# Performance work log

Measured on AMD Instinct MI355X. Metric: run time of the kernel, lower is better.

## Reference

```python
import jax, jax.numpy as jnp
import numpy as np

BEV_RANGE = 32.0   # meters; traj xy normalized to [-1,1] by this half-range
NUM_HEADS = 8
EGO_FUT_TS = 8
EPS = 1e-5


def _ln(x, g, b):
    m = x.mean(-1, keepdims=True)
    v = ((x - m) ** 2).mean(-1, keepdims=True)
    return (x - m) / jnp.sqrt(v + EPS) * g + b


def _mha(q, k, v, wq, bq, wk, bk, wv, bv, wo, bo):
    B, Lq, D = q.shape
    Lk = k.shape[1]
    dh = D // NUM_HEADS
    qh = (q @ wq + bq).reshape(B, Lq, NUM_HEADS, dh).transpose(0, 2, 1, 3)
    kh = (k @ wk + bk).reshape(B, Lk, NUM_HEADS, dh).transpose(0, 2, 1, 3)
    vh = (v @ wv + bv).reshape(B, Lk, NUM_HEADS, dh).transpose(0, 2, 1, 3)
    a = jax.nn.softmax(jnp.einsum('bhqd,bhkd->bhqk', qh, kh) * (1.0 / float(np.sqrt(dh))), axis=-1)
    o = jnp.einsum('bhqk,bhkd->bhqd', a, vh).transpose(0, 2, 1, 3).reshape(B, Lq, D)
    return o @ wo + bo


def _grid_sample(value, grid):
    # value (B,C,H,W); grid (B,M,P,2) xy in [-1,1]; bilinear, zeros padding, align_corners=False
    B, C, H, W = value.shape
    x = (grid[..., 0] + 1.0) * (W * 0.5) - 0.5
    y = (grid[..., 1] + 1.0) * (H * 0.5) - 0.5
    x0 = jnp.floor(x)
    y0 = jnp.floor(y)
    bidx = jnp.arange(B)[:, None, None]

    def corner(xi, yi, w):
        valid = (xi >= 0) & (xi <= W - 1) & (yi >= 0) & (yi <= H - 1)
        xc = jnp.clip(xi, 0, W - 1).astype(jnp.int32)
        yc = jnp.clip(yi, 0, H - 1).astype(jnp.int32)
        v = value[bidx, :, yc, xc]  # advanced idx -> (B,M,P,C)
        return v * (w * valid)[..., None]

    return (corner(x0, y0, (x0 + 1 - x) * (y0 + 1 - y))
            + corner(x0 + 1, y0, (x - x0) * (y0 + 1 - y))
            + corner(x0, y0 + 1, (x0 + 1 - x) * (y - y0))
            + corner(x0 + 1, y0 + 1, (x - x0) * (y - y0)))


def _mish(x):
    return x * jnp.tanh(jax.nn.softplus(x))


def _forward(traj_feature, noisy_traj_points, bev_feature, agents_query, ego_query,
             time_embed, status_encoding,
             bev_value_w, bev_value_b, bev_attn_w, bev_attn_b, bev_out_w, bev_out_b,
             aq_wq, aq_bq, aq_wk, aq_bk, aq_wv, aq_bv, aq_wo, aq_bo,
             eq_wq, eq_bq, eq_wk, eq_bk, eq_wv, eq_bv, eq_wo, eq_bo,
             ffn_w1, ffn_b1, ffn_w2, ffn_b2,
             n1_g, n1_b, n2_g, n2_b, n3_g, n3_b,
             mod_w, mod_b,
             cls_w1, cls_b1, cls_ln1_g, cls_ln1_b, cls_w2, cls_b2, cls_ln2_g, cls_ln2_b, cls_w3, cls_b3,
             reg_w1, reg_b1, reg_w2, reg_b2, reg_w3, reg_b3):
    B, M, D = traj_feature.shape
    # --- GridSampleCrossBEVAttention ---
    value = jnp.einsum('bchw,cd->bdhw', bev_feature, bev_value_w) + bev_value_b[None, :, None, None]
    grid = noisy_traj_points / BEV_RANGE                    # (B,M,P,2) in [-1,1]
    sampled = _grid_sample(value, grid)                     # (B,M,P,D)
    pt_w = jax.nn.softmax(traj_feature @ bev_attn_w + bev_attn_b, axis=-1)  # (B,M,P)
    bev_out = jnp.einsum('bmpd,bmp->bmd', sampled, pt_w) @ bev_out_w + bev_out_b
    traj = traj_feature + bev_out
    # --- cross-agent attention + norm1 ---
    traj = _ln(traj + _mha(traj, agents_query, agents_query,
                           aq_wq, aq_bq, aq_wk, aq_bk, aq_wv, aq_bv, aq_wo, aq_bo), n1_g, n1_b)
    # --- cross-ego attention + norm2 ---
    traj = _ln(traj + _mha(traj, ego_query, ego_query,
                           eq_wq, eq_bq, eq_wk, eq_bk, eq_wv, eq_bv, eq_wo, eq_bo), n2_g, n2_b)
    # --- FFN + norm3 (note: no residual, matches source) ---
    traj = _ln(jax.nn.relu(traj @ ffn_w1 + ffn_b1) @ ffn_w2 + ffn_b2, n3_g, n3_b)
    # --- FiLM time modulation ---
    ss = _mish(time_embed) @ mod_w + mod_b                  # (B,1,2D)
    scale, shift = jnp.split(ss, 2, axis=-1)
    traj = traj * (1.0 + scale) + shift
    # --- task decoder: cls branch (linear_relu_ln x2 + Linear->1) ---
    h = _ln(jax.nn.relu(traj @ cls_w1 + cls_b1), cls_ln1_g, cls_ln1_b)
    h = _ln(jax.nn.relu(h @ cls_w2 + cls_b2), cls_ln2_g, cls_ln2_b)
    plan_cls = (h @ cls_w3 + cls_b3)[..., 0]                # (B,M)
    # --- task decoder: reg branch ---
    r = jax.nn.relu(traj @ reg_w1 + reg_b1)
    r = jax.nn.relu(r @ reg_w2 + reg_b2)
    r = (r @ reg_w3 + reg_b3).reshape(B, M, EGO_FUT_TS, 3)
    xy = r[..., :2] + noisy_traj_points
    heading = jnp.tanh(r[..., 2:3]) * np.pi
    poses_reg = jnp.concatenate([xy, heading], axis=-1)     # (B,M,T,3)
    return poses_reg, plan_cls


def setup_inputs() -> dict:
    key = jax.random.key(0)
    ks = iter(jax.random.split(key, 80))
    rn = lambda *s: jax.random.normal(next(ks), s, dtype=jnp.float32)
    w = lambda *s: rn(*s) * 0.05
    B, M, P, D, A, FF = 32, 20, 8, 256, 32, 1024
    inp = dict(
        traj_feature=rn(B, M, D),
        noisy_traj_points=rn(B, M, P, 2) * 8.0,
        bev_feature=rn(B, 256, 128, 128),
        agents_query=rn(B, A, D),
        ego_query=rn(B, 1, D),
        time_embed=rn(B, 1, D),
        status_encoding=rn(B, 1, D),
        bev_value_w=w(256, D), bev_value_b=jnp.zeros(D),
        bev_attn_w=w(D, P), bev_attn_b=jnp.zeros(P),
        bev_out_w=w(D, D), bev_out_b=jnp.zeros(D),
        aq_wq=w(D, D), aq_bq=jnp.zeros(D), aq_wk=w(D, D), aq_bk=jnp.zeros(D),
        aq_wv=w(D, D), aq_bv=jnp.zeros(D), aq_wo=w(D, D), aq_bo=jnp.zeros(D),
        eq_wq=w(D, D), eq_bq=jnp.zeros(D), eq_wk=w(D, D), eq_bk=jnp.zeros(D),
        eq_wv=w(D, D), eq_bv=jnp.zeros(D), eq_wo=w(D, D), eq_bo=jnp.zeros(D),
        ffn_w1=w(D, FF), ffn_b1=jnp.zeros(FF), ffn_w2=w(FF, D), ffn_b2=jnp.zeros(D),
        n1_g=jnp.ones(D), n1_b=jnp.zeros(D), n2_g=jnp.ones(D), n2_b=jnp.zeros(D),
        n3_g=jnp.ones(D), n3_b=jnp.zeros(D),
        mod_w=w(D, 2 * D), mod_b=jnp.zeros(2 * D),
        cls_w1=w(D, D), cls_b1=jnp.zeros(D), cls_ln1_g=jnp.ones(D), cls_ln1_b=jnp.zeros(D),
        cls_w2=w(D, D), cls_b2=jnp.zeros(D), cls_ln2_g=jnp.ones(D), cls_ln2_b=jnp.zeros(D),
        cls_w3=w(D, 1), cls_b3=jnp.full((1,), float(-np.log((1 - 0.01) / 0.01))),
        reg_w1=w(D, D), reg_b1=jnp.zeros(D), reg_w2=w(D, D), reg_b2=jnp.zeros(D),
        reg_w3=w(D, EGO_FUT_TS * 3), reg_b3=jnp.zeros(EGO_FUT_TS * 3),
        bev_spatial_shape=jnp.array([128, 128], dtype=jnp.int32),
    )
    return inp


def reference(traj_feature, noisy_traj_points, bev_feature, agents_query, ego_query,
              time_embed, status_encoding,
              bev_value_w, bev_value_b, bev_attn_w, bev_attn_b, bev_out_w, bev_out_b,
              aq_wq, aq_bq, aq_wk, aq_bk, aq_wv, aq_bv, aq_wo, aq_bo,
              eq_wq, eq_bq, eq_wk, eq_bk, eq_wv, eq_bv, eq_wo, eq_bo,
              ffn_w1, ffn_b1, ffn_w2, ffn_b2,
              n1_g, n1_b, n2_g, n2_b, n3_g, n3_b,
              mod_w, mod_b,
              cls_w1, cls_b1, cls_ln1_g, cls_ln1_b, cls_w2, cls_b2, cls_ln2_g, cls_ln2_b, cls_w3, cls_b3,
              reg_w1, reg_b1, reg_w2, reg_b2, reg_w3, reg_b3,
              bev_spatial_shape):
    # bev_spatial_shape is implied by bev_feature's static shape under jit
    return _forward(traj_feature, noisy_traj_points, bev_feature, agents_query, ego_query,
                    time_embed, status_encoding,
                    bev_value_w, bev_value_b, bev_attn_w, bev_attn_b, bev_out_w, bev_out_b,
                    aq_wq, aq_bq, aq_wk, aq_bk, aq_wv, aq_bv, aq_wo, aq_bo,
                    eq_wq, eq_bq, eq_wk, eq_bk, eq_wv, eq_bv, eq_wo, eq_bo,
                    ffn_w1, ffn_b1, ffn_w2, ffn_b2,
                    n1_g, n1_b, n2_g, n2_b, n3_g, n3_b,
                    mod_w, mod_b,
                    cls_w1, cls_b1, cls_ln1_g, cls_ln1_b, cls_w2, cls_b2, cls_ln2_g, cls_ln2_b, cls_w3, cls_b3,
                    reg_w1, reg_b1, reg_w2, reg_b2, reg_w3, reg_b3)
```

## Files before the change

### kernel.cpp

```cpp
#include <hip/hip_runtime.h>
#include <math.h>

constexpr int NB = 32;
constexpr int NM = 20;
constexpr int NP = 8;
constexpr int ND = 256;
constexpr int NA = 32;
constexpr int NFF = 1024;
constexpr int NH = 128, NW = 128;
constexpr int HW = NH * NW;

constexpr int PK_BVW = 0;
constexpr int PK_BOW = 65536;
constexpr int PK_WQ  = 131072;
constexpr int PK_WO  = 196608;
constexpr int PK_CW1 = 262144;
constexpr int PK_CW2 = 327680;
constexpr int PK_RW1 = 393216;
constexpr int PK_RW2 = 458752;
constexpr int PK_FW1 = 655360;
constexpr int PK_FW2 = 917504;
constexpr int PK_ELEMS = 1048576;

constexpr int WS_GW   = 0;
constexpr int WS_WSUM = 163840;
constexpr int WS_K1   = 164480;
constexpr int WS_V1   = 426624;
constexpr int WS_U    = 688768;
constexpr int WS_SS   = 696960;
constexpr int WS_PACK = 720896;

__device__ __forceinline__ void dec2(unsigned u, float& f0, float& f1) {
    union { unsigned x; float f; } a, b;
    a.x = u << 16;
    b.x = u & 0xffff0000u;
    f0 = a.f; f1 = b.f;
}

__device__ __forceinline__ float fma4(float4 a, uint2 w, float acc) {
    float w0, w1, w2, w3;
    dec2(w.x, w0, w1);
    dec2(w.y, w2, w3);
    acc += a.x * w0;
    acc += a.y * w1;
    acc += a.z * w2;
    acc += a.w * w3;
    return acc;
}

__device__ __forceinline__ float gemm256(const uint2* __restrict__ wp, const float* __restrict__ sa,
                                         int t, float acc) {
    const float4* a4 = (const float4*)sa;
    #pragma unroll 8
    for (int c4 = 0; c4 < 64; ++c4) {
        float4 a = a4[c4];
        uint2 w = wp[(c4 << 8) + t];
        acc = fma4(a, w, acc);
    }
    return acc;
}

constexpr int GB_GATHER = NB * NM;
constexpr int GB_KV     = NB * NA / 4;
constexpr int GB_PERB   = NB;
constexpr int GB_PACK   = PK_ELEMS / 256;
constexpr int PRO_GRID  = GB_GATHER + GB_KV + GB_PERB + GB_PACK;

struct PackArgs {
    const float* src[10];
    int log2N[10];
    int elems[10];
    int dstoff[10];
};

struct ProArgs {
    const float *traj, *noisy, *bev, *attn_w, *attn_b;
    const float *agents, *wk, *bk, *wv, *bv;
    const float *ego, *eq_wv, *eq_bv, *eq_wo, *eq_bo;
    const float *temb, *modw, *modb;
    float *gw, *wsum, *K1, *V1, *u, *ss;
    unsigned short* pk;
};

__global__ void prologue_kernel(ProArgs A, PackArgs pa) {
    int blk = blockIdx.x, tid = threadIdx.x;
    __shared__ __align__(16) float sm0[ND];
    __shared__ __align__(16) float sm1[ND];
    __shared__ __align__(16) float sm2[ND];
    __shared__ __align__(16) float sm3[ND];
    __shared__ float s_ptw[NP];
    __shared__ float s_w[32];
    __shared__ int s_idx[32];

    if (blk < GB_GATHER) {
        int b = blk / NM;
        sm0[tid] = A.traj[(size_t)blk * ND + tid];
        __syncthreads();
        if (tid < NP) {
            float acc = A.attn_b[tid];
            for (int c = 0; c < ND; c++) acc += sm0[c] * A.attn_w[c * NP + tid];
            s_ptw[tid] = acc;
        }
        __syncthreads();
        if (tid == 0) {
            float mx = s_ptw[0];
            for (int p = 1; p < NP; p++) mx = fmaxf(mx, s_ptw[p]);
            float e[NP], sum = 0.f;
            for (int p = 0; p < NP; p++) { e[p] = expf(s_ptw[p] - mx); sum += e[p]; }
            for (int p = 0; p < NP; p++) s_ptw[p] = e[p] / sum;
        }
        __syncthreads();
        if (tid < 32) {
            int p = tid >> 2, corner = tid & 3;
            float gx = A.noisy[((size_t)blk * NP + p) * 2 + 0] * (1.0f / 32.0f);
            float gy = A.noisy[((size_t)blk * NP + p) * 2 + 1] * (1.0f / 32.0f);
            float x = (gx + 1.0f) * (NW * 0.5f) - 0.5f;
            float y = (gy + 1.0f) * (NH * 0.5f) - 0.5f;
            float x0 = floorf(x), y0 = floorf(y);
            int dx = corner & 1, dy = corner >> 1;
            float wx = dx ? (x - x0) : (x0 + 1.0f - x);
            float wy = dy ? (y - y0) : (y0 + 1.0f - y);
            float xi = x0 + (float)dx, yi = y0 + (float)dy;
            bool valid = (xi >= 0.f) && (xi <= (float)(NW - 1)) && (yi >= 0.f) && (yi <= (float)(NH - 1));
            int xc = (int)fminf(fmaxf(xi, 0.f), (float)(NW - 1));
            int yc = (int)fminf(fmaxf(yi, 0.f), (float)(NH - 1));
            s_w[tid] = wx * wy * (valid ? 1.f : 0.f) * s_ptw[p];
            s_idx[tid] = yc * NW + xc;
        }
        __syncthreads();
        if (tid == 0) {
            float s = 0.f;
            for (int j = 0; j < 32; j++) s += s_w[j];
            A.wsum[blk] = s;
        }
        const float* base = A.bev + (size_t)b * ND * HW + (size_t)tid * HW;
        float acc0 = 0.f, acc1 = 0.f;
        #pragma unroll
        for (int j = 0; j < 32; j += 2) {
            acc0 += s_w[j]     * base[s_idx[j]];
            acc1 += s_w[j + 1] * base[s_idx[j + 1]];
        }
        A.gw[(size_t)blk * ND + tid] = acc0 + acc1;
    } else if (blk < GB_GATHER + GB_KV) {
        int a0 = (blk - GB_GATHER) * 4;
        sm0[tid] = A.agents[(size_t)a0 * ND + tid];
        sm1[tid] = A.agents[(size_t)(a0 + 1) * ND + tid];
        sm2[tid] = A.agents[(size_t)(a0 + 2) * ND + tid];
        sm3[tid] = A.agents[(size_t)(a0 + 3) * ND + tid];
        __syncthreads();
        float k0 = A.bk[tid], k1 = k0, k2 = k0, k3 = k0;
        float v0 = A.bv[tid], v1 = v0, v2 = v0, v3 = v0;
        #pragma unroll 4
        for (int c = 0; c < ND; ++c) {
            float wk = A.wk[(size_t)c * ND + tid];
            float wv = A.wv[(size_t)c * ND + tid];
            float a0f = sm0[c], a1f = sm1[c], a2f = sm2[c], a3f = sm3[c];
            k0 += a0f * wk; k1 += a1f * wk; k2 += a2f * wk; k3 += a3f * wk;
            v0 += a0f * wv; v1 += a1f * wv; v2 += a2f * wv; v3 += a3f * wv;
        }
        A.K1[(size_t)a0 * ND + tid] = k0;
        A.K1[(size_t)(a0 + 1) * ND + tid] = k1;
        A.K1[(size_t)(a0 + 2) * ND + tid] = k2;
        A.K1[(size_t)(a0 + 3) * ND + tid] = k3;
        A.V1[(size_t)a0 * ND + tid] = v0;
        A.V1[(size_t)(a0 + 1) * ND + tid] = v1;
        A.V1[(size_t)(a0 + 2) * ND + tid] = v2;
        A.V1[(size_t)(a0 + 3) * ND + tid] = v3;
    } else if (blk < GB_GATHER + GB_KV + GB_PERB) {
        int b = blk - (GB_GATHER + GB_KV);
        sm0[tid] = A.ego[(size_t)b * ND + tid];
        __syncthreads();
        float v = A.eq_bv[tid];
        for (int c = 0; c < ND; c++) v += sm0[c] * A.eq_wv[c * ND + tid];
        sm1[tid] = v;
        __syncthreads();
        float o = A.eq_bo[tid];
        for (int c = 0; c < ND; c++) o += sm1[c] * A.eq_wo[c * ND + tid];
        A.u[(size_t)b * ND + tid] = o;

        float te = A.temb[(size_t)b * ND + tid];
        float sp = log1pf(expf(te));
        float me = te * tanhf(sp);
        __syncthreads();
        sm0[tid] = me;
        __syncthreads();
        for (int jj = 0; jj < 2; jj++) {
            int j = tid + jj * ND;
            float acc = A.modb[j];
            for (int c = 0; c < ND; c++) acc += sm0[c] * A.modw[(size_t)c * 2 * ND + j];
            A.ss[(size_t)b * 2 * ND + j] = acc;
        }
    } else {
        int e = (blk - (GB_GATHER + GB_KV + GB_PERB)) * 256 + tid;
        int seg = 0;
        while (seg < 10 && e >= pa.elems[seg]) { e -= pa.elems[seg]; seg++; }
        if (seg < 10) {
            int lg = pa.log2N[seg];
            int N = 1 << lg;
            int c = e >> lg;
            int n = e & (N - 1);
            float v = pa.src[seg][e];
            union { float f; unsigned u; } uu; uu.f = v;
            unsigned x = uu.u;
            unsigned r = (x + 0x7fff + ((x >> 16) & 1)) >> 16;
            int idx = (((c >> 2) << lg) + n) * 4 + (c & 3);
            A.pk[pa.dstoff[seg] + idx] = (unsigned short)r;
        }
    }
}

__device__ __forceinline__ float half_sum(float v, float* s_red, int tid) {
    for (int off = 32; off > 0; off >>= 1) v += __shfl_down(v, off, 64);
    __syncthreads();
    if ((tid & 63) == 0) s_red[tid >> 6] = v;
    __syncthreads();
    int base = (tid >> 8) << 2;
    return s_red[base] + s_red[base + 1] + s_red[base + 2] + s_red[base + 3];
}

__device__ __forceinline__ float half_ln(float x, const float* g, const float* bb, float* s_red, int tid) {
    int t = tid & 255;
    float mean = half_sum(x, s_red, tid) * (1.0f / 256.0f);
    float xm = x - mean;
    float var = half_sum(xm * xm, s_red, tid) * (1.0f / 256.0f);
    return xm / sqrtf(var + 1e-5f) * g[t] + bb[t];
}

struct MegaW {
    const float *traj, *noisy;
    const float *bvb, *bob, *bq, *bo;
    const float *n1g, *n1b, *n2g, *n2b;
    const float *fb1, *fb2, *n3g, *n3b;
    const float *cb1, *cl1g, *cl1b, *cb2, *cl2g, *cl2b, *cw3, *cb3;
    const float *rb1, *rb2, *rw3, *rb3;
};

__global__ __launch_bounds__(512, 4)
void mega_kernel(const float* __restrict__ gw, const float* __restrict__ wsumw,
                 const float* __restrict__ K1, const float* __restrict__ V1,
                 const float* __restrict__ u, const float* __restrict__ ss,
                 const uint2* __restrict__ bvwp, const uint2* __restrict__ bowp,
                 const uint2* __restrict__ wqp, const uint2* __restrict__ wop,
                 const uint2* __restrict__ fw1p, const uint2* __restrict__ fw2p,
                 const uint2* __restrict__ cw1p, const uint2* __restrict__ cw2p,
                 const uint2* __restrict__ rw1p, const uint2* __restrict__ rw2p,
                 MegaW W, float* __restrict__ out) {
    int blk = blockIdx.x;
    int tid = threadIdx.x;
    int half = tid >> 8;
    int t = tid & 255;
    int tok = blk * 2 + half;
    int b = tok / NM;
    __shared__ __align__(16) float s_a[2][ND];
    __shared__ __align__(16) float s_b[2][ND];
    __shared__ __align__(16) float s_h[2][NFF];
    __shared__ __align__(16) float s_sc[2][ND];
    __shared__ float s_red[8];

    s_sc[half][t] = gw[(size_t)tok * ND + t];
    float wsw = wsumw[tok];
    __syncthreads();
    float acc = gemm256(bvwp, s_sc[half], t, W.bvb[t] * wsw);
    __syncthreads();
    s_b[half][t] = acc;
    __syncthreads();
    acc = gemm256(bowp, s_b[half], t, W.bob[t] + W.traj[(size_t)tok * ND + t]);
    s_a[half][t] = acc;
    __syncthreads();
    acc = gemm256(wqp, s_a[half], t, W.bq[t]);
    __syncthreads();
    s_b[half][t] = acc;
    __syncthreads();
    int h = t >> 5, kk = t & 31;
    {
        const float* Krow = K1 + ((size_t)(b * NA + kk)) * ND + h * 32;
        float sc = 0.f;
        for (int j = 0; j < 32; j++) sc += s_b[half][h * 32 + j] * Krow[j];
        s_sc[half][t] = sc * 0.17677669529663687f;
    }
    __syncthreads();
    {
        float mx = -1e30f;
        for (int j = 0; j < 32; j++) mx = fmaxf(mx, s_sc[half][h * 32 + j]);
        float den = 0.f;
        for (int j = 0; j < 32; j++) den += expf(s_sc[half][h * 32 + j] - mx);
        float p = expf(s_sc[half][t] - mx) / den;
        __syncthreads();
        s_sc[half][t] = p;
        __syncthreads();
    }
    {
        const float* Vb = V1 + (size_t)b * NA * ND;
        float o = 0.f;
        for (int k = 0; k < 32; k++) o += s_sc[half][h * 32 + k] * Vb[(size_t)k * ND + t];
        __syncthreads();
        s_b[half][t] = o;
        __syncthreads();
    }
    acc = gemm256(wop, s_b[half], t, W.bo[t] + s_a[half][t]);
    float t1 = half_ln(acc, W.n1g, W.n1b, s_red, tid);
    float t2 = half_ln(t1 + u[(size_t)b * ND + t], W.n2g, W.n2b, s_red, tid);
    __syncthreads();
    s_a[half][t] = t2;
    __syncthreads();
    {
        float f0 = W.fb1[t], f1 = W.fb1[t + 256], f2 = W.fb1[t + 512], f3 = W.fb1[t + 768];
        const float4* a4 = (const float4*)s_a[half];
        #pragma unroll 4
        for (int c4 = 0; c4 < 64; ++c4) {
            float4 a = a4[c4];
            f0 = fma4(a, fw1p[(c4 << 10) + t], f0);
            f1 = fma4(a, fw1p[(c4 << 10) + 256 + t], f1);
            f2 = fma4(a, fw1p[(c4 << 10) + 512 + t], f2);
            f3 = fma4(a, fw1p[(c4 << 10) + 768 + t], f3);
        }
        s_h[half][t] = fmaxf(f0, 0.f);
        s_h[half][t + 256] = fmaxf(f1, 0.f);
        s_h[half][t + 512] = fmaxf(f2, 0.f);
        s_h[half][t + 768] = fmaxf(f3, 0.f);
    }
    __syncthreads();
    {
        acc = W.fb2[t];
        const float4* h4 = (const float4*)s_h[half];
        #pragma unroll 8
        for (int c4 = 0; c4 < 256; ++c4) {
            acc = fma4(h4[c4], fw2p[(c4 << 8) + t], acc);
        }
    }
    float t3 = half_ln(acc, W.n3g, W.n3b, s_red, tid);
    float sc1 = ss[(size_t)b * 2 * ND + t];
    float sh1 = ss[(size_t)b * 2 * ND + ND + t];
    float tt = t3 * (1.f + sc1) + sh1;
    __syncthreads();
    s_a[half][t] = tt;
    __syncthreads();
    acc = gemm256(cw1p, s_a[half], t, W.cb1[t]);
    float h1 = half_ln(fmaxf(acc, 0.f), W.cl1g, W.cl1b, s_red, tid);
    __syncthreads();
    s_b[half][t] = h1;
    __syncthreads();
    acc = gemm256(cw2p, s_b[half], t, W.cb2[t]);
    float h2 = half_ln(fmaxf(acc, 0.f), W.cl2g, W.cl2b, s_red, tid);
    float pc = half_sum(h2 * W.cw3[t], s_red, tid);
    if (t == 0) out[(size_t)NB * NM * NP * 3 + tok] = pc + W.cb3[0];
    acc = gemm256(rw1p, s_a[half], t, W.rb1[t]);
    __syncthreads();
    s_b[half][t] = fmaxf(acc, 0.f);
    __syncthreads();
    acc = gemm256(rw2p, s_b[half], t, W.rb2[t]);
    __syncthreads();
    s_b[half][t] = fmaxf(acc, 0.f);
    __syncthreads();
    if (t < 24) {
        float r3 = W.rb3[t];
        for (int c = 0; c < ND; c++) r3 += s_b[half][c] * W.rw3[c * 24 + t];
        int ts = t / 3, k2 = t % 3;
        float val;
        if (k2 < 2) val = r3 + W.noisy[((size_t)tok * NP + ts) * 2 + k2];
        else        val = tanhf(r3) * 3.14159265358979323846f;
        out[((size_t)tok * NP + ts) * 3 + k2] = val;
    }
}

extern "C" void kernel_launch(void* const* d_in, const int* in_sizes, int n_in,
                              void* d_out, int out_size, void* d_ws, size_t ws_size,
                              hipStream_t stream) {
    const float* traj   = (const float*)d_in[0];
    const float* noisy  = (const float*)d_in[1];
    const float* bev    = (const float*)d_in[2];
    const float* agents = (const float*)d_in[3];
    const float* ego    = (const float*)d_in[4];
    const float* temb   = (const float*)d_in[5];
    const float* bvw = (const float*)d_in[7];
    const float* bvb = (const float*)d_in[8];
    const float* baw = (const float*)d_in[9];
    const float* bab = (const float*)d_in[10];
    const float* bow = (const float*)d_in[11];
    const float* bob = (const float*)d_in[12];
    const float* aq_wq = (const float*)d_in[13];
    const float* aq_bq = (const float*)d_in[14];
    const float* aq_wk = (const float*)d_in[15];
    const float* aq_bk = (const float*)d_in[16];
    const float* aq_wv = (const float*)d_in[17];
    const float* aq_bv = (const float*)d_in[18];
    const float* aq_wo = (const float*)d_in[19];
    const float* aq_bo = (const float*)d_in[20];
    const float* eq_wv = (const float*)d_in[25];
    const float* eq_bv = (const float*)d_in[26];
    const float* eq_wo = (const float*)d_in[27];
    const float* eq_bo = (const float*)d_in[28];
    const float* fw1 = (const float*)d_in[29];
    const float* fb1 = (const float*)d_in[30];
    const float* fw2 = (const float*)d_in[31];
    const float* fb2 = (const float*)d_in[32];
    const float* n1g = (const float*)d_in[33];
    const float* n1b = (const float*)d_in[34];
    const float* n2g = (const float*)d_in[35];
    const float* n2b = (const float*)d_in[36];
    const float* n3g = (const float*)d_in[37];
    const float* n3b = (const float*)d_in[38];
    const float* modw = (const float*)d_in[39];
    const float* modb = (const float*)d_in[40];
    const float* cw1 = (const float*)d_in[41];
    const float* cb1 = (const float*)d_in[42];
    const float* cl1g = (const float*)d_in[43];
    const float* cl1b = (const float*)d_in[44];
    const float* cw2 = (const float*)d_in[45];
    const float* cb2 = (const float*)d_in[46];
    const float* cl2g = (const float*)d_in[47];
    const float* cl2b = (const float*)d_in[48];
    const float* cw3 = (const float*)d_in[49];
    const float* cb3 = (const float*)d_in[50];
    const float* rw1 = (const float*)d_in[51];
    const float* rb1 = (const float*)d_in[52];
    const float* rw2 = (const float*)d_in[53];
    const float* rb2 = (const float*)d_in[54];
    const float* rw3 = (const float*)d_in[55];
    const float* rb3 = (const float*)d_in[56];

    float* ws = (float*)d_ws;
    float* gw    = ws + WS_GW;
    float* wsumw = ws + WS_WSUM;
    float* K1    = ws + WS_K1;
    float* V1    = ws + WS_V1;
    float* u     = ws + WS_U;
    float* ssb   = ws + WS_SS;
    unsigned short* pk = (unsigned short*)(ws + WS_PACK);

    PackArgs pa;
    const float* srcs[10] = {bvw, bow, aq_wq, aq_wo, cw1, cw2, rw1, rw2, fw1, fw2};
    int lg[10]  = {8, 8, 8, 8, 8, 8, 8, 8, 10, 8};
    int el[10]  = {65536, 65536, 65536, 65536, 65536, 65536, 65536, 65536, 262144, 262144};
    int off[10] = {PK_BVW, PK_BOW, PK_WQ, PK_WO, PK_CW1, PK_CW2, PK_RW1, PK_RW2, PK_FW1, PK_FW2};
    for (int i = 0; i < 10; i++) { pa.src[i] = srcs[i]; pa.log2N[i] = lg[i]; pa.elems[i] = el[i]; pa.dstoff[i] = off[i]; }

    ProArgs PA;
    PA.traj = traj; PA.noisy = noisy; PA.bev = bev; PA.attn_w = baw; PA.attn_b = bab;
    PA.agents = agents; PA.wk = aq_wk; PA.bk = aq_bk; PA.wv = aq_wv; PA.bv = aq_bv;
    PA.ego = ego; PA.eq_wv = eq_wv; PA.eq_bv = eq_bv; PA.eq_wo = eq_wo; PA.eq_bo = eq_bo;
    PA.temb = temb; PA.modw = modw; PA.modb = modb;
    PA.gw = gw; PA.wsum = wsumw; PA.K1 = K1; PA.V1 = V1; PA.u = u; PA.ss = ssb;
    PA.pk = pk;

    prologue_kernel<<<dim3(PRO_GRID), dim3(256), 0, stream>>>(PA, pa);

    MegaW W;
    W.traj = traj; W.noisy = noisy;
    W.bvb = bvb; W.bob = bob; W.bq = aq_bq; W.bo = aq_bo;
    W.n1g = n1g; W.n1b = n1b; W.n2g = n2g; W.n2b = n2b;
    W.fb1 = fb1; W.fb2 = fb2; W.n3g = n3g; W.n3b = n3b;
    W.cb1 = cb1; W.cl1g = cl1g; W.cl1b = cl1b;
    W.cb2 = cb2; W.cl2g = cl2g; W.cl2b = cl2b; W.cw3 = cw3; W.cb3 = cb3;
    W.rb1 = rb1; W.rb2 = rb2; W.rw3 = rw3; W.rb3 = rb3;

    mega_kernel<<<dim3(NB * NM / 2), dim3(512), 0, stream>>>(gw, wsumw, K1, V1, u, ssb,
        (const uint2*)(pk + PK_BVW), (const uint2*)(pk + PK_BOW),
        (const uint2*)(pk + PK_WQ),  (const uint2*)(pk + PK_WO),
        (const uint2*)(pk + PK_FW1), (const uint2*)(pk + PK_FW2),
        (const uint2*)(pk + PK_CW1), (const uint2*)(pk + PK_CW2),
        (const uint2*)(pk + PK_RW1), (const uint2*)(pk + PK_RW2),
        W, (float*)d_out);
}
```

Baseline: 875.3 us.

## Process two tokens per thread in mega kernel to reuse decoded bf16 weights

Each half-block now handles two tokens at once, with activations stored as float2 in shared memory, so every packed bf16 weight load and decode feeds two FMAs instead of one. The grid is halved to 160 blocks and the launch-bounds occupancy hint drops from 4 to 2 to leave room for more registers. Weight bandwidth per token is halved, but fewer blocks on a 256-CU part leaves many CUs idle and lowers latency hiding. The batch index is taken from the first token of the block, which stays correct because 20 tokens per batch divide evenly by 4.

```diff
diff --git a/kernel.cpp b/kernel.cpp
--- a/kernel.cpp
+++ b/kernel.cpp
@@ -37,6 +37,12 @@
     f0 = a.f; f1 = b.f;
 }
 
+__device__ __forceinline__ float2 pk_fma(float2 a, float w, float2 acc) {
+    acc.x = fmaf(a.x, w, acc.x);
+    acc.y = fmaf(a.y, w, acc.y);
+    return acc;
+}
+
 __device__ __forceinline__ float fma4(float4 a, uint2 w, float acc) {
     float w0, w1, w2, w3;
     dec2(w.x, w0, w1);
@@ -48,14 +54,21 @@
     return acc;
 }
 
-__device__ __forceinline__ float gemm256(const uint2* __restrict__ wp, const float* __restrict__ sa,
-                                         int t, float acc) {
-    const float4* a4 = (const float4*)sa;
+__device__ __forceinline__ float2 gemm256x2(const uint2* __restrict__ wp, const float2* __restrict__ sa2,
+                                            int t, float2 acc) {
+    const float4* a4 = (const float4*)sa2;
     #pragma unroll 8
     for (int c4 = 0; c4 < 64; ++c4) {
-        float4 a = a4[c4];
+        float4 p = a4[c4 * 2];
+        float4 q = a4[c4 * 2 + 1];
         uint2 w = wp[(c4 << 8) + t];
-        acc = fma4(a, w, acc);
+        float w0, w1, w2, w3;
+        dec2(w.x, w0, w1);
+        dec2(w.y, w2, w3);
+        acc = pk_fma(make_float2(p.x, p.y), w0, acc);
+        acc = pk_fma(make_float2(p.z, p.w), w1, acc);
+        acc = pk_fma(make_float2(q.x, q.y), w2, acc);
+        acc = pk_fma(make_float2(q.z, q.w), w3, acc);
     }
     return acc;
 }
@@ -209,21 +222,33 @@
     }
 }
 
-__device__ __forceinline__ float half_sum(float v, float* s_red, int tid) {
-    for (int off = 32; off > 0; off >>= 1) v += __shfl_down(v, off, 64);
-    __syncthreads();
-    if ((tid & 63) == 0) s_red[tid >> 6] = v;
+__device__ __forceinline__ float2 half_sum2(float2 v, float2* s_red2, int tid) {
+    for (int off = 32; off > 0; off >>= 1) {
+        v.x += __shfl_down(v.x, off, 64);
+        v.y += __shfl_down(v.y, off, 64);
+    }
+    __syncthreads();
+    if ((tid & 63) == 0) s_red2[tid >> 6] = v;
     __syncthreads();
     int base = (tid >> 8) << 2;
-    return s_red[base] + s_red[base + 1] + s_red[base + 2] + s_red[base + 3];
-}
-
-__device__ __forceinline__ float half_ln(float x, const float* g, const float* bb, float* s_red, int tid) {
+    float2 r;
+    r.x = s_red2[base].x + s_red2[base + 1].x + s_red2[base + 2].x + s_red2[base + 3].x;
+    r.y = s_red2[base].y + s_red2[base + 1].y + s_red2[base + 2].y + s_red2[base + 3].y;
+    return r;
+}
+
+__device__ __forceinline__ float2 half_ln2(float2 x, const float* g, const float* bb, float2* s_red2, int tid) {
     int t = tid & 255;
-    float mean = half_sum(x, s_red, tid) * (1.0f / 256.0f);
-    float xm = x - mean;
-    float var = half_sum(xm * xm, s_red, tid) * (1.0f / 256.0f);
-    return xm / sqrtf(var + 1e-5f) * g[t] + bb[t];
+    float2 mean = half_sum2(x, s_red2, tid);
+    mean.x *= (1.0f / 256.0f);
+    mean.y *= (1.0f / 256.0f);
+    float2 xm = make_float2(x.x - mean.x, x.y - mean.y);
+    float2 var = half_sum2(make_float2(xm.x * xm.x, xm.y * xm.y), s_red2, tid);
+    var.x *= (1.0f / 256.0f);
+    var.y *= (1.0f / 256.0f);
+    float gg = g[t], bbf = bb[t];
+    return make_float2(xm.x / sqrtf(var.x + 1e-5f) * gg + bbf,
+                       xm.y / sqrtf(var.y + 1e-5f) * gg + bbf);
 }
 
 struct MegaW {
@@ -235,7 +260,7 @@
     const float *rb1, *rb2, *rw3, *rb3;
 };
 
-__global__ __launch_bounds__(512, 4)
+__global__ __launch_bounds__(512, 2)
 void mega_kernel(const float* __restrict__ gw, const float* __restrict__ wsumw,
                  const float* __restrict__ K1, const float* __restrict__ V1,
                  const float* __restrict__ u, const float* __restrict__ ss,
@@ -249,117 +274,179 @@
     int tid = threadIdx.x;
     int half = tid >> 8;
     int t = tid & 255;
-    int tok = blk * 2 + half;
-    int b = tok / NM;
-    __shared__ __align__(16) float s_a[2][ND];
-    __shared__ __align__(16) float s_b[2][ND];
-    __shared__ __align__(16) float s_h[2][NFF];
-    __shared__ __align__(16) float s_sc[2][ND];
-    __shared__ float s_red[8];
-
-    s_sc[half][t] = gw[(size_t)tok * ND + t];
-    float wsw = wsumw[tok];
-    __syncthreads();
-    float acc = gemm256(bvwp, s_sc[half], t, W.bvb[t] * wsw);
-    __syncthreads();
-    s_b[half][t] = acc;
-    __syncthreads();
-    acc = gemm256(bowp, s_b[half], t, W.bob[t] + W.traj[(size_t)tok * ND + t]);
-    s_a[half][t] = acc;
-    __syncthreads();
-    acc = gemm256(wqp, s_a[half], t, W.bq[t]);
-    __syncthreads();
-    s_b[half][t] = acc;
+    int tok0 = blk * 4;
+    int tokA = tok0 + half * 2;
+    int tokB = tokA + 1;
+    int b = tok0 / NM;
+    __shared__ __align__(16) float2 s_a2[2][ND];
+    __shared__ __align__(16) float2 s_b2[2][ND];
+    __shared__ __align__(16) float2 s_sc2[2][ND];
+    __shared__ __align__(16) float2 s_h2[2][NFF];
+    __shared__ float2 s_red2[8];
+
+    s_sc2[half][t] = make_float2(gw[(size_t)tokA * ND + t], gw[(size_t)tokB * ND + t]);
+    float wsA = wsumw[tokA], wsB = wsumw[tokB];
+    __syncthreads();
+    float bvbt = W.bvb[t];
+    float2 acc2 = gemm256x2(bvwp, s_sc2[half], t, make_float2(bvbt * wsA, bvbt * wsB));
+    __syncthreads();
+    s_b2[half][t] = acc2;
+    __syncthreads();
+    float bobt = W.bob[t];
+    acc2 = gemm256x2(bowp, s_b2[half], t,
+                     make_float2(bobt + W.traj[(size_t)tokA * ND + t],
+                                 bobt + W.traj[(size_t)tokB * ND + t]));
+    s_a2[half][t] = acc2;
+    __syncthreads();
+    float bqt = W.bq[t];
+    acc2 = gemm256x2(wqp, s_a2[half], t, make_float2(bqt, bqt));
+    __syncthreads();
+    s_b2[half][t] = acc2;
     __syncthreads();
     int h = t >> 5, kk = t & 31;
     {
         const float* Krow = K1 + ((size_t)(b * NA + kk)) * ND + h * 32;
-        float sc = 0.f;
-        for (int j = 0; j < 32; j++) sc += s_b[half][h * 32 + j] * Krow[j];
-        s_sc[half][t] = sc * 0.17677669529663687f;
+        const float2* qrow = s_b2[half] + h * 32;
+        float2 sc = make_float2(0.f, 0.f);
+        for (int j = 0; j < 32; j++) sc = pk_fma(qrow[j], Krow[j], sc);
+        s_sc2[half][t] = make_float2(sc.x * 0.17677669529663687f, sc.y * 0.17677669529663687f);
     }
     __syncthreads();
     {
-        float mx = -1e30f;
-        for (int j = 0; j < 32; j++) mx = fmaxf(mx, s_sc[half][h * 32 + j]);
-        float den = 0.f;
-        for (int j = 0; j < 32; j++) den += expf(s_sc[half][h * 32 + j] - mx);
-        float p = expf(s_sc[half][t] - mx) / den;
-        __syncthreads();
-        s_sc[half][t] = p;
+        const float2* scrow = s_sc2[half] + h * 32;
+        float2 mx = make_float2(-1e30f, -1e30f);
+        for (int j = 0; j < 32; j++) {
+            mx.x = fmaxf(mx.x, scrow[j].x);
+            mx.y = fmaxf(mx.y, scrow[j].y);
+        }
+        float2 den = make_float2(0.f, 0.f);
+        for (int j = 0; j < 32; j++) {
+            den.x += expf(scrow[j].x - mx.x);
+            den.y += expf(scrow[j].y - mx.y);
+        }
+        float2 me = s_sc2[half][t];
+        float2 p = make_float2(expf(me.x - mx.x) / den.x, expf(me.y - mx.y) / den.y);
+        __syncthreads();
+        s_sc2[half][t] = p;
         __syncthreads();
     }
     {
         const float* Vb = V1 + (size_t)b * NA * ND;
-        float o = 0.f;
-        for (int k = 0; k < 32; k++) o += s_sc[half][h * 32 + k] * Vb[(size_t)k * ND + t];
-        __syncthreads();
-        s_b[half][t] = o;
-        __syncthreads();
-    }
-    acc = gemm256(wop, s_b[half], t, W.bo[t] + s_a[half][t]);
-    float t1 = half_ln(acc, W.n1g, W.n1b, s_red, tid);
-    float t2 = half_ln(t1 + u[(size_t)b * ND + t], W.n2g, W.n2b, s_red, tid);
-    __syncthreads();
-    s_a[half][t] = t2;
+        const float2* prow = s_sc2[half] + h * 32;
+        float2 o = make_float2(0.f, 0.f);
+        for (int k = 0; k < 32; k++) o = pk_fma(prow[k], Vb[(size_t)k * ND + t], o);
+        __syncthreads();
+        s_b2[half][t] = o;
+        __syncthreads();
+    }
+    float bot = W.bo[t];
+    acc2 = gemm256x2(wop, s_b2[half], t,
+                     make_float2(bot + s_a2[half][t].x, bot + s_a2[half][t].y));
+    float2 t1 = half_ln2(acc2, W.n1g, W.n1b, s_red2, tid);
+    float uu = u[(size_t)b * ND + t];
+    float2 t2 = half_ln2(make_float2(t1.x + uu, t1.y + uu), W.n2g, W.n2b, s_red2, tid);
+    __syncthreads();
+    s_a2[half][t] = t2;
     __syncthreads();
     {
-        float f0 = W.fb1[t], f1 = W.fb1[t + 256], f2 = W.fb1[t + 512], f3 = W.fb1[t + 768];
-        const float4* a4 = (const float4*)s_a[half];
+        float b0 = W.fb1[t], b1 = W.fb1[t + 256], b2 = W.fb1[t + 512], b3 = W.fb1[t + 768];
+        float2 f0 = make_float2(b0, b0), f1 = make_float2(b1, b1);
+        float2 f2 = make_float2(b2, b2), f3 = make_float2(b3, b3);
+        const float4* a4 = (const float4*)s_a2[half];
         #pragma unroll 4
         for (int c4 = 0; c4 < 64; ++c4) {
-            float4 a = a4[c4];
-            f0 = fma4(a, fw1p[(c4 << 10) + t], f0);
-            f1 = fma4(a, fw1p[(c4 << 10) + 256 + t], f1);
-            f2 = fma4(a, fw1p[(c4 << 10) + 512 + t], f2);
-            f3 = fma4(a, fw1p[(c4 << 10) + 768 + t], f3);
-        }
-        s_h[half][t] = fmaxf(f0, 0.f);
-        s_h[half][t + 256] = fmaxf(f1, 0.f);
-        s_h[half][t + 512] = fmaxf(f2, 0.f);
-        s_h[half][t + 768] = fmaxf(f3, 0.f);
+            float4 p = a4[c4 * 2];
+            float4 q = a4[c4 * 2 + 1];
+            float2 a0 = make_float2(p.x, p.y), a1 = make_float2(p.z, p.w);
+            float2 a2 = make_float2(q.x, q.y), a3 = make_float2(q.z, q.w);
+            uint2 w; float w0, w1, w2, w3;
+            w = fw1p[(c4 << 10) + t];
+            dec2(w.x, w0, w1); dec2(w.y, w2, w3);
+            f0 = pk_fma(a0, w0, f0); f0 = pk_fma(a1, w1, f0);
+            f0 = pk_fma(a2, w2, f0); f0 = pk_fma(a3, w3, f0);
+            w = fw1p[(c4 << 10) + 256 + t];
+            dec2(w.x, w0, w1); dec2(w.y, w2, w3);
+            f1 = pk_fma(a0, w0, f1); f1 = pk_fma(a1, w1, f1);
+            f1 = pk_fma(a2, w2, f1); f1 = pk_fma(a3, w3, f1);
+            w = fw1p[(c4 << 10) + 512 + t];
+            dec2(w.x, w0, w1); dec2(w.y, w2, w3);
+            f2 = pk_fma(a0, w0, f2); f2 = pk_fma(a1, w1, f2);
+            f2 = pk_fma(a2, w2, f2); f2 = pk_fma(a3, w3, f2);
+            w = fw1p[(c4 << 10) + 768 + t];
+            dec2(w.x, w0, w1); dec2(w.y, w2, w3);
+            f3 = pk_fma(a0, w0, f3); f3 = pk_fma(a1, w1, f3);
+            f3 = pk_fma(a2, w2, f3); f3 = pk_fma(a3, w3, f3);
+        }
+        s_h2[half][t]       = make_float2(fmaxf(f0.x, 0.f), fmaxf(f0.y, 0.f));
+        s_h2[half][t + 256] = make_float2(fmaxf(f1.x, 0.f), fmaxf(f1.y, 0.f));
+        s_h2[half][t + 512] = make_float2(fmaxf(f2.x, 0.f), fmaxf(f2.y, 0.f));
+        s_h2[half][t + 768] = make_float2(fmaxf(f3.x, 0.f), fmaxf(f3.y, 0.f));
     }
     __syncthreads();
     {
-        acc = W.fb2[t];
-        const float4* h4 = (const float4*)s_h[half];
+        float fb2t = W.fb2[t];
+        acc2 = make_float2(fb2t, fb2t);
+        const float4* h4 = (const float4*)s_h2[half];
         #pragma unroll 8
         for (int c4 = 0; c4 < 256; ++c4) {
-            acc = fma4(h4[c4], fw2p[(c4 << 8) + t], acc);
-        }
-    }
-    float t3 = half_ln(acc, W.n3g, W.n3b, s_red, tid);
+            float4 p = h4[c4 * 2];
+            float4 q = h4[c4 * 2 + 1];
+            uint2 w = fw2p[(c4 << 8) + t];
+            float w0, w1, w2, w3;
+            dec2(w.x, w0, w1); dec2(w.y, w2, w3);
+            acc2 = pk_fma(make_float2(p.x, p.y), w0, acc2);
+            acc2 = pk_fma(make_float2(p.z, p.w), w1, acc2);
+            acc2 = pk_fma(make_float2(q.x, q.y), w2, acc2);
+            acc2 = pk_fma(make_float2(q.z, q.w), w3, acc2);
+        }
+    }
+    float2 t3 = half_ln2(acc2, W.n3g, W.n3b, s_red2, tid);
     float sc1 = ss[(size_t)b * 2 * ND + t];
     float sh1 = ss[(size_t)b * 2 * ND + ND + t];
-    float tt = t3 * (1.f + sc1) + sh1;
-    __syncthreads();
-    s_a[half][t] = tt;
-    __syncthreads();
-    acc = gemm256(cw1p, s_a[half], t, W.cb1[t]);
-    float h1 = half_ln(fmaxf(acc, 0.f), W.cl1g, W.cl1b, s_red, tid);
-    __syncthreads();
-    s_b[half][t] = h1;
-    __syncthreads();
-    acc = gemm256(cw2p, s_b[half], t, W.cb2[t]);
-    float h2 = half_ln(fmaxf(acc, 0.f), W.cl2g, W.cl2b, s_red, tid);
-    float pc = half_sum(h2 * W.cw3[t], s_red, tid);
-    if (t == 0) out[(size_t)NB * NM * NP * 3 + tok] = pc + W.cb3[0];
-    acc = gemm256(rw1p, s_a[half], t, W.rb1[t]);
-    __syncthreads();
-    s_b[half][t] = fmaxf(acc, 0.f);
-    __syncthreads();
-    acc = gemm256(rw2p, s_b[half], t, W.rb2[t]);
-    __syncthreads();
-    s_b[half][t] = fmaxf(acc, 0.f);
+    float2 tt = make_float2(t3.x * (1.f + sc1) + sh1, t3.y * (1.f + sc1) + sh1);
+    __syncthreads();
+    s_a2[half][t] = tt;
+    __syncthreads();
+    float cb1t = W.cb1[t];
+    acc2 = gemm256x2(cw1p, s_a2[half], t, make_float2(cb1t, cb1t));
+    float2 h1 = half_ln2(make_float2(fmaxf(acc2.x, 0.f), fmaxf(acc2.y, 0.f)),
+                         W.cl1g, W.cl1b, s_red2, tid);
+    __syncthreads();
+    s_b2[half][t] = h1;
+    __syncthreads();
+    float cb2t = W.cb2[t];
+    acc2 = gemm256x2(cw2p, s_b2[half], t, make_float2(cb2t, cb2t));
+    float2 h2v = half_ln2(make_float2(fmaxf(acc2.x, 0.f), fmaxf(acc2.y, 0.f)),
+                          W.cl2g, W.cl2b, s_red2, tid);
+    float cw3t = W.cw3[t];
+    float2 pc = half_sum2(make_float2(h2v.x * cw3t, h2v.y * cw3t), s_red2, tid);
+    if (t == 0) {
+        out[(size_t)NB * NM * NP * 3 + tokA] = pc.x + W.cb3[0];
+        out[(size_t)NB * NM * NP * 3 + tokB] = pc.y + W.cb3[0];
+    }
+    float rb1t = W.rb1[t];
+    acc2 = gemm256x2(rw1p, s_a2[half], t, make_float2(rb1t, rb1t));
+    __syncthreads();
+    s_b2[half][t] = make_float2(fmaxf(acc2.x, 0.f), fmaxf(acc2.y, 0.f));
+    __syncthreads();
+    float rb2t = W.rb2[t];
+    acc2 = gemm256x2(rw2p, s_b2[half], t, make_float2(rb2t, rb2t));
+    __syncthreads();
+    s_b2[half][t] = make_float2(fmaxf(acc2.x, 0.f), fmaxf(acc2.y, 0.f));
     __syncthreads();
     if (t < 24) {
-        float r3 = W.rb3[t];
-        for (int c = 0; c < ND; c++) r3 += s_b[half][c] * W.rw3[c * 24 + t];
+        float rb3t = W.rb3[t];
+        float2 r3 = make_float2(rb3t, rb3t);
+        const float2* sb = s_b2[half];
+        for (int c = 0; c < ND; c++) r3 = pk_fma(sb[c], W.rw3[c * 24 + t], r3);
         int ts = t / 3, k2 = t % 3;
-        float val;
-        if (k2 < 2) val = r3 + W.noisy[((size_t)tok * NP + ts) * 2 + k2];
-        else        val = tanhf(r3) * 3.14159265358979323846f;
-        out[((size_t)tok * NP + ts) * 3 + k2] = val;
+        if (k2 < 2) {
+            out[((size_t)tokA * NP + ts) * 3 + k2] = r3.x + W.noisy[((size_t)tokA * NP + ts) * 2 + k2];
+            out[((size_t)tokB * NP + ts) * 3 + k2] = r3.y + W.noisy[((size_t)tokB * NP + ts) * 2 + k2];
+        } else {
+            out[((size_t)tokA * NP + ts) * 3 + k2] = tanhf(r3.x) * 3.14159265358979323846f;
+            out[((size_t)tokB * NP + ts) * 3 + k2] = tanhf(r3.y) * 3.14159265358979323846f;
+        }
     }
 }
 
@@ -454,7 +541,7 @@
     W.cb2 = cb2; W.cl2g = cl2g; W.cl2b = cl2b; W.cw3 = cw3; W.cb3 = cb3;
     W.rb1 = rb1; W.rb2 = rb2; W.rw3 = rw3; W.rb3 = rb3;
 
-    mega_kernel<<<dim3(NB * NM / 2), dim3(512), 0, stream>>>(gw, wsumw, K1, V1, u, ssb,
+    mega_kernel<<<dim3(NB * NM / 4), dim3(512), 0, stream>>>(gw, wsumw, K1, V1, u, ssb,
         (const uint2*)(pk + PK_BVW), (const uint2*)(pk + PK_BOW),
         (const uint2*)(pk + PK_WQ),  (const uint2*)(pk + PK_WO),
         (const uint2*)(pk + PK_FW1), (const uint2*)(pk + PK_FW2),
```

Measured after the change: 831.6 us. 5.0% less time.
